# Kernel tuning notes

Measured on AMD Instinct MI355X. Metric: run time of the kernel, lower is better.

Reference implementation:

```python
import jax, jax.numpy as jnp
import numpy as np

B, L, H, C = 32, 2048, 512, 50
KERNEL = 3  # avgpool kernel, stride 1, pad 1, count_include_pad=False


def _avgpool3_no_pad_count(x):
    """AvgPool1d(kernel=3, stride=1, pad=1, count_include_pad=False) along last axis.
    x: (..., L). Zero-pad, sum 3-tap windows, divide by number of valid elements."""
    pad = [(0, 0)] * (x.ndim - 1) + [(1, 1)]
    xp = jnp.pad(x, pad)
    s = xp[..., :-2] + xp[..., 1:-1] + xp[..., 2:]
    ones = jnp.pad(jnp.ones_like(x), pad)
    cnt = ones[..., :-2] + ones[..., 1:-1] + ones[..., 2:]
    return s / cnt


def setup_inputs() -> dict:
    key = jax.random.key(0)
    k1, k2, k3, k4, k5, k6 = jax.random.split(key, 6)
    sent_keys = jax.random.normal(k1, (B, L, H), dtype=jnp.float32)
    sent_values = jax.random.normal(k2, (B, L, H), dtype=jnp.float32)
    sent_lens = jax.random.randint(k3, (B,), 1, L + 1).astype(jnp.int64)
    W1 = jax.random.normal(k4, (H, H), dtype=jnp.float32) * 0.02
    W2 = jax.random.normal(k5, (H, H), dtype=jnp.float32) * 0.02
    W3 = jax.random.normal(k6, (C, H), dtype=jnp.float32) * 0.02
    return {"sent_keys": sent_keys, "sent_values": sent_values,
            "sent_lens": sent_lens, "W1": W1, "W2": W2, "W3": W3}


def reference(sent_keys, sent_values, sent_lens, W1, W2, W3):
    # Tiny MLP scorer (dropout is identity in eval mode)
    p1 = jnp.tanh(jnp.einsum('blh,kh->blk', sent_keys, W1))   # (B,L,H)
    p2 = jnp.tanh(jnp.einsum('blh,kh->blk', p1, W2))          # (B,L,H)
    p3 = jnp.einsum('blh,ch->blc', p1 + p2, W3)               # (B,L,C)

    b, l, c = p3.shape
    # Fill padded positions with the score at the last valid position (index len-1)
    last_idx = (sent_lens - 1).astype(jnp.int32)[:, None, None]        # (B,1,1)
    last = jnp.take_along_axis(p3, jnp.broadcast_to(last_idx, (b, 1, c)), axis=1)  # (B,1,C)
    mask = (jnp.arange(l)[None, :] < sent_lens[:, None])[:, :, None]   # (B,L,1)
    kq = jnp.where(mask, p3, last)

    # Smooth along doc-position axis with avgpool(count_include_pad=False)
    smoothened_kq = _avgpool3_no_pad_count(kq.transpose(0, 2, 1)).transpose(0, 2, 1)  # (B,L,C)

    # Softmax over classes, then zero out padded positions
    attention_values = jax.nn.softmax(smoothened_kq, axis=2)
    attention_values = jnp.where(mask, attention_values, 0.0)

    # (B,C,L) @ (B,L,H) -> (B,C,H)
    class_inputs = jnp.einsum('blc,blh->bch', attention_values, sent_values)
    return attention_values, class_inputs, smoothened_kq
```

## Files before the change

### kernel.cpp

```cpp
#include <hip/hip_runtime.h>
#include <cstdint>

#define Bc 32
#define Lc 2048
#define Hc 512
#define Cc 50
#define PCc 52
#define Mc (Bc*Lc)

typedef short s8v   __attribute__((ext_vector_type(8)));
typedef float f4v   __attribute__((ext_vector_type(4)));

__device__ inline unsigned short f2bf(float f) {
    unsigned int u = __float_as_uint(f);
    u += 0x7fffu + ((u >> 16) & 1u);
    return (unsigned short)(u >> 16);
}
__device__ inline float bf2f(unsigned short h) {
    return __uint_as_float(((unsigned int)h) << 16);
}
__device__ inline float fast_tanh(float x) {
    float e = __expf(2.0f * x);
    return 1.0f - 2.0f / (e + 1.0f);
}
__device__ inline void gl_lds16(const unsigned short* g, unsigned short* l) {
    __builtin_amdgcn_global_load_lds(
        (const __attribute__((address_space(1))) unsigned int*)g,
        (__attribute__((address_space(3))) unsigned int*)l, 16, 0, 0);
}

__global__ __launch_bounds__(256)
void f32_to_bf16_kernel(const float* __restrict__ in, unsigned short* __restrict__ out)
{
    size_t i = ((size_t)blockIdx.x * 256 + threadIdx.x) * 8;
    float4 a = *(const float4*)(in + i);
    float4 b = *(const float4*)(in + i + 4);
    s8v o;
    o[0]=f2bf(a.x); o[1]=f2bf(a.y); o[2]=f2bf(a.z); o[3]=f2bf(a.w);
    o[4]=f2bf(b.x); o[5]=f2bf(b.y); o[6]=f2bf(b.z); o[7]=f2bf(b.w);
    *(s8v*)(out + i) = o;
}

__global__ __launch_bounds__(256)
void convert_weights_kernel(const float* __restrict__ W1, const float* __restrict__ W2,
                            const float* __restrict__ W3,
                            unsigned short* __restrict__ W1b,
                            unsigned short* __restrict__ W2b,
                            unsigned short* __restrict__ W3b)
{
    int e = (blockIdx.x * 256 + threadIdx.x) * 8;
    if (e >= 524288) {
        int off = e - 524288;
        int row = off >> 9;
        s8v o;
        #pragma unroll
        for (int j = 0; j < 8; ++j)
            o[j] = (row < Cc) ? (short)f2bf(W3[off + j]) : (short)0;
        *(s8v*)(W3b + off) = o;
        return;
    }
    const float* src = (e < 262144) ? W1 : W2;
    unsigned short* dst = (e < 262144) ? W1b : W2b;
    int off = (e < 262144) ? e : e - 262144;
    float4 a = *(const float4*)(src + off);
    float4 b = *(const float4*)(src + off + 4);
    s8v o;
    o[0]=f2bf(a.x); o[1]=f2bf(a.y); o[2]=f2bf(a.z); o[3]=f2bf(a.w);
    o[4]=f2bf(b.x); o[5]=f2bf(b.y); o[6]=f2bf(b.z); o[7]=f2bf(b.w);
    *(s8v*)(dst + off) = o;
}

__global__ __launch_bounds__(256)
void transpose_v_kernel(const float* __restrict__ V, unsigned short* __restrict__ Vt)
{
    __shared__ float tile[64 * 65];
    const int l0 = blockIdx.x * 64;
    const int h0 = blockIdx.y * 64;
    const int b  = blockIdx.z;
    const int tid = threadIdx.x;
    const int li = tid >> 2;
    const int hq = (tid & 3) * 4;

    const float* src = V + ((size_t)(b * Lc + l0 + li)) * Hc + h0 + hq;
    #pragma unroll
    for (int j = 0; j < 4; ++j) {
        float4 v = *(const float4*)(src + 16 * j);
        float* d = &tile[li * 65 + hq + 16 * j];
        d[0] = v.x; d[1] = v.y; d[2] = v.z; d[3] = v.w;
    }
    __syncthreads();

    const int lane = tid & 63;
    const int w4   = tid >> 6;
    const int lpos = (lane & 15) * 4;
    #pragma unroll
    for (int i = 0; i < 4; ++i) {
        int hr = i * 16 + w4 * 4 + (lane >> 4);
        ushort4 o;
        o.x = f2bf(tile[(lpos + 0) * 65 + hr]);
        o.y = f2bf(tile[(lpos + 1) * 65 + hr]);
        o.z = f2bf(tile[(lpos + 2) * 65 + hr]);
        o.w = f2bf(tile[(lpos + 3) * 65 + hr]);
        *(ushort4*)(Vt + ((size_t)(b * Hc + h0 + hr)) * Lc + l0 + lpos) = o;
    }
}

__global__ __launch_bounds__(256)
void mfma_gemm512(const unsigned short* __restrict__ Ab,
                  const unsigned short* __restrict__ Wb,
                  unsigned short* __restrict__ Ob, int mode)
{
    __shared__ alignas(16) char smem[32768];
    float* Esf = (float*)smem;

    const int tid = threadIdx.x;
    const int w = tid >> 6, l = tid & 63;

    const int bid = blockIdx.x;
    const int ixd = bid >> 3;
    const int y   = (bid & 7) * 64 + (ixd >> 2);
    const int x   = ixd & 3;
    const int j0 = x * 128;
    const int i0 = y * 128;

    const int sr  = w * 16 + (l >> 2);
    const int kg8 = (l & 3) * 8;
    const unsigned short* Ag0 = Ab + (size_t)(i0 + sr) * 512 + kg8;
    const unsigned short* Ag1 = Ag0 + (size_t)64 * 512;
    const unsigned short* Bg0 = Wb + (size_t)(j0 + sr) * 512 + kg8;
    const unsigned short* Bg1 = Bg0 + (size_t)64 * 512;

    const int wm = (w & 1) * 64, wn = (w >> 1) * 64;
    const int fr = l & 15;
    const int fq = (l >> 4) * 8;

    f4v acc[4][4];
    #pragma unroll
    for (int r = 0; r < 4; ++r)
        #pragma unroll
        for (int c = 0; c < 4; ++c) acc[r][c] = (f4v){0.f, 0.f, 0.f, 0.f};

    auto STAGE = [&](int buf, int k0) {
        unsigned short* a = (unsigned short*)(smem + buf * 16384);
        unsigned short* b = (unsigned short*)(smem + 8192 + buf * 16384);
        gl_lds16(Ag0 + k0, a + w * 512);
        gl_lds16(Ag1 + k0, a + 2048 + w * 512);
        gl_lds16(Bg0 + k0, b + w * 512);
        gl_lds16(Bg1 + k0, b + 2048 + w * 512);
    };
    auto COMPUTE = [&](int buf) {
        const unsigned short* a = (const unsigned short*)(smem + buf * 16384);
        const unsigned short* b = (const unsigned short*)(smem + 8192 + buf * 16384);
        s8v af[4], bv[4];
        #pragma unroll
        for (int r = 0; r < 4; ++r)
            af[r] = *(const s8v*)&a[(wm + r * 16 + fr) * 32 + fq];
        #pragma unroll
        for (int c = 0; c < 4; ++c)
            bv[c] = *(const s8v*)&b[(wn + c * 16 + fr) * 32 + fq];
        #pragma unroll
        for (int r = 0; r < 4; ++r)
            #pragma unroll
            for (int c = 0; c < 4; ++c)
                acc[r][c] = __builtin_amdgcn_mfma_f32_16x16x32_bf16(
                    af[r], bv[c], acc[r][c], 0, 0, 0);
    };

    STAGE(0, 0);
    #pragma unroll
    for (int t = 0; t < 15; ++t) {
        STAGE((t + 1) & 1, (t + 1) * 32);
        asm volatile("s_waitcnt vmcnt(4)" ::: "memory");
        __builtin_amdgcn_s_barrier();
        COMPUTE(t & 1);
        asm volatile("s_waitcnt lgkmcnt(0)" ::: "memory");
        __builtin_amdgcn_s_barrier();
    }
    asm volatile("s_waitcnt vmcnt(0)" ::: "memory");
    __builtin_amdgcn_s_barrier();
    COMPUTE(1);
    asm volatile("s_waitcnt lgkmcnt(0)" ::: "memory");
    __builtin_amdgcn_s_barrier();

    #pragma unroll
    for (int h = 0; h < 4; ++h) {
        if (h) __syncthreads();
        if ((w & 1) == (h >> 1)) {
            const int rr = (h & 1) * 2;
            #pragma unroll
            for (int r = 0; r < 2; ++r)
                #pragma unroll
                for (int c = 0; c < 4; ++c)
                    #pragma unroll
                    for (int v = 0; v < 4; ++v) {
                        int row = r * 16 + (l >> 4) * 4 + v;
                        int col = wn + c * 16 + fr;
                        Esf[row * 133 + col] = fast_tanh(acc[rr + r][c][v]);
                    }
        }
        __syncthreads();
        #pragma unroll
        for (int t = 0; t < 4; ++t) {
            int chunk = t * 256 + tid;
            int row = chunk >> 5;
            int c4  = (chunk & 31) * 4;
            f4v val = *(const f4v*)&Esf[row * 133 + c4];
            size_t gr   = (size_t)(i0 + (h >> 1) * 64 + (h & 1) * 32 + row);
            size_t goff = gr * 512 + j0 + c4;
            ushort4 o;
            if (mode) {
                ushort4 a = *(const ushort4*)(Ab + goff);
                o.x = f2bf(val[0] + bf2f(a.x));
                o.y = f2bf(val[1] + bf2f(a.y));
                o.z = f2bf(val[2] + bf2f(a.z));
                o.w = f2bf(val[3] + bf2f(a.w));
            } else {
                o.x = f2bf(val[0]); o.y = f2bf(val[1]);
                o.z = f2bf(val[2]); o.w = f2bf(val[3]);
            }
            *(ushort4*)(Ob + goff) = o;
        }
    }
}

__global__ __launch_bounds__(256)
void mfma_gemm_p3(const unsigned short* __restrict__ Sb,
                  const unsigned short* __restrict__ W3b,
                  float* __restrict__ P3)
{
    __shared__ alignas(16) char smem[24576];
    const int tid = threadIdx.x;
    const int w = tid >> 6, l = tid & 63;
    const int i0 = blockIdx.x * 128;

    const int sr  = w * 16 + (l >> 2);
    const int kg8 = (l & 3) * 8;
    const unsigned short* Ag0 = Sb + (size_t)(i0 + sr) * 512 + kg8;
    const unsigned short* Ag1 = Ag0 + (size_t)64 * 512;
    const unsigned short* Bg  = W3b + (size_t)sr * 512 + kg8;

    const int wm = w * 32;
    const int fr = l & 15;
    const int fq = (l >> 4) * 8;

    f4v acc[2][4];
    #pragma unroll
    for (int r = 0; r < 2; ++r)
        #pragma unroll
        for (int c = 0; c < 4; ++c) acc[r][c] = (f4v){0.f, 0.f, 0.f, 0.f};

    auto STAGE = [&](int buf, int k0) {
        unsigned short* a = (unsigned short*)(smem + buf * 12288);
        unsigned short* b = (unsigned short*)(smem + 8192 + buf * 12288);
        gl_lds16(Ag0 + k0, a + w * 512);
        gl_lds16(Ag1 + k0, a + 2048 + w * 512);
        gl_lds16(Bg  + k0, b + w * 512);
    };
    auto COMPUTE = [&](int buf) {
        const unsigned short* a = (const unsigned short*)(smem + buf * 12288);
        const unsigned short* b = (const unsigned short*)(smem + 8192 + buf * 12288);
        s8v af[2], bv[4];
        #pragma unroll
        for (int r = 0; r < 2; ++r)
            af[r] = *(const s8v*)&a[(wm + r * 16 + fr) * 32 + fq];
        #pragma unroll
        for (int c = 0; c < 4; ++c)
            bv[c] = *(const s8v*)&b[(c * 16 + fr) * 32 + fq];
        #pragma unroll
        for (int r = 0; r < 2; ++r)
            #pragma unroll
            for (int c = 0; c < 4; ++c)
                acc[r][c] = __builtin_amdgcn_mfma_f32_16x16x32_bf16(
                    af[r], bv[c], acc[r][c], 0, 0, 0);
    };

    STAGE(0, 0);
    #pragma unroll
    for (int t = 0; t < 15; ++t) {
        STAGE((t + 1) & 1, (t + 1) * 32);
        asm volatile("s_waitcnt vmcnt(3)" ::: "memory");
        __builtin_amdgcn_s_barrier();
        COMPUTE(t & 1);
        asm volatile("s_waitcnt lgkmcnt(0)" ::: "memory");
        __builtin_amdgcn_s_barrier();
    }
    asm volatile("s_waitcnt vmcnt(0)" ::: "memory");
    __builtin_amdgcn_s_barrier();
    COMPUTE(1);

    #pragma unroll
    for (int r = 0; r < 2; ++r)
        #pragma unroll
        for (int v = 0; v < 4; ++v) {
            const int row = i0 + wm + r * 16 + (l >> 4) * 4 + v;
            #pragma unroll
            for (int c = 0; c < 4; ++c) {
                const int col = c * 16 + fr;
                if (col < Cc) P3[(size_t)row * PCc + col] = acc[r][c][v];
            }
        }
}

__global__ __launch_bounds__(64)
void normalize_lens_kernel(const int* __restrict__ raw, int* __restrict__ lens)
{
    __shared__ int is64;
    if (threadIdx.x == 0) {
        int orv = 0;
        for (int i = 1; i < 32; i += 2) orv |= raw[i];
        is64 = (orv == 0) ? 1 : 0;
    }
    __syncthreads();
    int b = threadIdx.x;
    if (b < Bc) lens[b] = is64 ? raw[2*b] : raw[b];
}

__global__ __launch_bounds__(256)
void pool_softmax_kernel(const float* __restrict__ P3, const int* __restrict__ lens,
                         float* __restrict__ out_attn, float* __restrict__ out_smooth,
                         unsigned short* __restrict__ attnT)
{
    const int idx = blockIdx.x * 256 + threadIdx.x;
    const int b = idx >> 11;
    const int l = idx & (Lc - 1);
    const int len = lens[b];
    const float* base = P3 + (size_t)b * Lc * PCc;

    const int  r0 = min(l, len - 1);
    const bool hm = (l > 0);
    const bool hp = (l < Lc - 1);
    const int  rm = hm ? min(l - 1, len - 1) : 0;
    const int  rp = hp ? min(l + 1, len - 1) : 0;
    const float rcnt = 1.f / (1.f + (hm ? 1.f : 0.f) + (hp ? 1.f : 0.f));

    float sm[PCc];
    const float* p0 = base + (size_t)r0 * PCc;
    #pragma unroll
    for (int q = 0; q < 13; ++q) {
        f4v v = *(const f4v*)(p0 + q * 4);
        sm[q*4+0] = v[0]; sm[q*4+1] = v[1]; sm[q*4+2] = v[2]; sm[q*4+3] = v[3];
    }
    if (hm) {
        const float* p = base + (size_t)rm * PCc;
        #pragma unroll
        for (int q = 0; q < 13; ++q) {
            f4v v = *(const f4v*)(p + q * 4);
            sm[q*4+0] += v[0]; sm[q*4+1] += v[1]; sm[q*4+2] += v[2]; sm[q*4+3] += v[3];
        }
    }
    if (hp) {
        const float* p = base + (size_t)rp * PCc;
        #pragma unroll
        for (int q = 0; q < 13; ++q) {
            f4v v = *(const f4v*)(p + q * 4);
            sm[q*4+0] += v[0]; sm[q*4+1] += v[1]; sm[q*4+2] += v[2]; sm[q*4+3] += v[3];
        }
    }

    float mx = -1e30f;
    #pragma unroll
    for (int c = 0; c < Cc; ++c) {
        sm[c] *= rcnt;
        mx = fmaxf(mx, sm[c]);
    }
    float* srow = out_smooth + (size_t)idx * Cc;
    #pragma unroll
    for (int q = 0; q < 25; ++q) {
        float2 v = make_float2(sm[q*2], sm[q*2+1]);
        *(float2*)(srow + q * 2) = v;
    }

    float sum = 0.f;
    #pragma unroll
    for (int c = 0; c < Cc; ++c) {
        float e = __expf(sm[c] - mx);
        sm[c] = e;
        sum += e;
    }
    const float inv = 1.f / sum;
    const bool valid = (l < len);
    const float scale = valid ? inv : 0.f;
    float* arow = out_attn + (size_t)idx * Cc;
    unsigned short* trow = attnT + (size_t)b * 64 * Lc + l;
    #pragma unroll
    for (int c = 0; c < Cc; ++c) sm[c] *= scale;
    #pragma unroll
    for (int q = 0; q < 25; ++q)
        *(float2*)(arow + q * 2) = make_float2(sm[q*2], sm[q*2+1]);
    #pragma unroll
    for (int c = 0; c < Cc; ++c)
        trow[(size_t)c * Lc] = f2bf(sm[c]);
}

__global__ __launch_bounds__(256)
void class_mfma_kernel(const unsigned short* __restrict__ attnT,
                       const unsigned short* __restrict__ Vt,
                       float* __restrict__ out_class)
{
    __shared__ alignas(16) unsigned short As[64 * 32];
    __shared__ alignas(16) unsigned short Bs[128 * 32];
    const int tid = threadIdx.x;
    const int w = tid >> 6, l = tid & 63;

    const int bid  = blockIdx.x;
    const int ixd  = bid >> 3;
    const int pair = (bid & 7) * 16 + (ixd >> 2);
    const int n0 = (ixd & 3) * 128;
    const int b  = pair >> 2;
    const int kb = (pair & 3) * 512;

    const int sr  = w * 16 + (l >> 2);
    const int kg8 = (l & 3) * 8;
    const unsigned short* Ag  = attnT + ((size_t)b * 64 + sr) * Lc + kg8;
    const unsigned short* Bg0 = Vt + ((size_t)(b * Hc + n0 + sr)) * Lc + kg8;
    const unsigned short* Bg1 = Bg0 + (size_t)64 * Lc;
    unsigned short* Al  = As + w * 512;
    unsigned short* Bl0 = Bs + w * 512;
    unsigned short* Bl1 = Bs + 2048 + w * 512;

    const int fr = l & 15;
    const int fq = (l >> 4) * 8;

    f4v acc[4][2];
    #pragma unroll
    for (int r = 0; r < 4; ++r)
        #pragma unroll
        for (int c = 0; c < 2; ++c) acc[r][c] = (f4v){0.f, 0.f, 0.f, 0.f};

    for (int k0 = kb; k0 < kb + 512; k0 += 32) {
        gl_lds16(Ag + k0, Al);
        gl_lds16(Bg0 + k0, Bl0);
        gl_lds16(Bg1 + k0, Bl1);
        __syncthreads();
        s8v af[4], bv[2];
        #pragma unroll
        for (int r = 0; r < 4; ++r)
            af[r] = *(const s8v*)&As[(r * 16 + fr) * 32 + fq];
        #pragma unroll
        for (int c = 0; c < 2; ++c)
            bv[c] = *(const s8v*)&Bs[(w * 32 + c * 16 + fr) * 32 + fq];
        #pragma unroll
        for (int r = 0; r < 4; ++r)
            #pragma unroll
            for (int c = 0; c < 2; ++c)
                acc[r][c] = __builtin_amdgcn_mfma_f32_16x16x32_bf16(
                    af[r], bv[c], acc[r][c], 0, 0, 0);
        __syncthreads();
    }

    #pragma unroll
    for (int r = 0; r < 4; ++r)
        #pragma unroll
        for (int v = 0; v < 4; ++v) {
            const int m = r * 16 + (l >> 4) * 4 + v;
            if (m < Cc) {
                #pragma unroll
                for (int c = 0; c < 2; ++c) {
                    const int h = n0 + w * 32 + c * 16 + fr;
                    atomicAdd(out_class + ((size_t)b * Cc + m) * Hc + h,
                              acc[r][c][v]);
                }
            }
        }
}

extern "C" void kernel_launch(void* const* d_in, const int* in_sizes, int n_in,
                              void* d_out, int out_size, void* d_ws, size_t ws_size,
                              hipStream_t stream)
{
    const float* keys     = (const float*)d_in[0];
    const float* vals     = (const float*)d_in[1];
    const int*   lens_raw = (const int*)d_in[2];
    const float* W1       = (const float*)d_in[3];
    const float* W2       = (const float*)d_in[4];
    const float* W3       = (const float*)d_in[5];

    char* ws = (char*)d_ws;
    const size_t MB = 1024 * 1024;
    unsigned short* Akv  = (unsigned short*)ws;
    float*          P3   = (float*)ws;
    unsigned short* P1b  = (unsigned short*)(ws + 64 * MB);
    unsigned short* Vt   = (unsigned short*)(ws + 64 * MB);
    unsigned short* Sb   = (unsigned short*)(ws + 128 * MB);
    unsigned short* W1b  = (unsigned short*)(ws + 192 * MB);
    unsigned short* W2b  = W1b + Hc * Hc;
    unsigned short* W3b  = W2b + Hc * Hc;
    unsigned short* attnT= (unsigned short*)(ws + 194 * MB);
    int*            lens = (int*)(ws + 202 * MB);

    float* out_attn   = (float*)d_out;
    float* out_class  = out_attn + (size_t)Bc * Lc * Cc;
    float* out_smooth = out_class + (size_t)Bc * Cc * Hc;

    hipMemsetAsync(out_class, 0, (size_t)Bc * Cc * Hc * sizeof(float), stream);

    f32_to_bf16_kernel<<<(Mc * Hc / 8) / 256, 256, 0, stream>>>(keys, Akv);
    convert_weights_kernel<<<272, 256, 0, stream>>>(W1, W2, W3, W1b, W2b, W3b);
    normalize_lens_kernel<<<1, 64, 0, stream>>>(lens_raw, lens);

    mfma_gemm512<<<2048, 256, 0, stream>>>(Akv, W1b, P1b, 0);
    mfma_gemm512<<<2048, 256, 0, stream>>>(P1b, W2b, Sb, 1);
    transpose_v_kernel<<<dim3(Lc / 64, Hc / 64, Bc), 256, 0, stream>>>(vals, Vt);
    mfma_gemm_p3<<<Mc / 128, 256, 0, stream>>>(Sb, W3b, P3);
    pool_softmax_kernel<<<Mc / 256, 256, 0, stream>>>(P3, lens, out_attn, out_smooth, attnT);
    class_mfma_kernel<<<512, 256, 0, stream>>>(attnT, Vt, out_class);
}
```

Baseline: 507.4 us.

## Replace double-buffered K pipeline with single-buffered 64-wide K steps in GEMMs

The two MLP GEMM kernels drop their hand-scheduled double-buffered pipeline (manual vmcnt/lgkmcnt waits and raw barriers). Each now loads a 64-wide K chunk as two 32-wide halves into one buffer, syncs, computes both halves, and syncs again. The class GEMM also moves from 32-wide to 64-wide K steps, halving its barrier count. This trades global-load/compute overlap in the MLP GEMMs for simpler code and fewer barriers per unit of K, and may expose load latency there.

```diff
diff --git a/kernel.cpp b/kernel.cpp
--- a/kernel.cpp
+++ b/kernel.cpp
@@ -111,6 +111,8 @@
                   unsigned short* __restrict__ Ob, int mode)
 {
     __shared__ alignas(16) char smem[32768];
+    unsigned short* As = (unsigned short*)smem;
+    unsigned short* Bs = (unsigned short*)(smem + 16384);
     float* Esf = (float*)smem;
 
     const int tid = threadIdx.x;
@@ -140,47 +142,33 @@
         #pragma unroll
         for (int c = 0; c < 4; ++c) acc[r][c] = (f4v){0.f, 0.f, 0.f, 0.f};
 
-    auto STAGE = [&](int buf, int k0) {
-        unsigned short* a = (unsigned short*)(smem + buf * 16384);
-        unsigned short* b = (unsigned short*)(smem + 8192 + buf * 16384);
-        gl_lds16(Ag0 + k0, a + w * 512);
-        gl_lds16(Ag1 + k0, a + 2048 + w * 512);
-        gl_lds16(Bg0 + k0, b + w * 512);
-        gl_lds16(Bg1 + k0, b + 2048 + w * 512);
-    };
-    auto COMPUTE = [&](int buf) {
-        const unsigned short* a = (const unsigned short*)(smem + buf * 16384);
-        const unsigned short* b = (const unsigned short*)(smem + 8192 + buf * 16384);
-        s8v af[4], bv[4];
-        #pragma unroll
-        for (int r = 0; r < 4; ++r)
-            af[r] = *(const s8v*)&a[(wm + r * 16 + fr) * 32 + fq];
-        #pragma unroll
-        for (int c = 0; c < 4; ++c)
-            bv[c] = *(const s8v*)&b[(wn + c * 16 + fr) * 32 + fq];
-        #pragma unroll
-        for (int r = 0; r < 4; ++r)
+    for (int k0 = 0; k0 < 512; k0 += 64) {
+        #pragma unroll
+        for (int h = 0; h < 2; ++h) {
+            gl_lds16(Ag0 + k0 + h * 32, As + h * 4096 + w * 512);
+            gl_lds16(Ag1 + k0 + h * 32, As + h * 4096 + 2048 + w * 512);
+            gl_lds16(Bg0 + k0 + h * 32, Bs + h * 4096 + w * 512);
+            gl_lds16(Bg1 + k0 + h * 32, Bs + h * 4096 + 2048 + w * 512);
+        }
+        __syncthreads();
+        #pragma unroll
+        for (int h = 0; h < 2; ++h) {
+            s8v af[4], bv[4];
+            #pragma unroll
+            for (int r = 0; r < 4; ++r)
+                af[r] = *(const s8v*)&As[h * 4096 + (wm + r * 16 + fr) * 32 + fq];
             #pragma unroll
             for (int c = 0; c < 4; ++c)
-                acc[r][c] = __builtin_amdgcn_mfma_f32_16x16x32_bf16(
-                    af[r], bv[c], acc[r][c], 0, 0, 0);
-    };
-
-    STAGE(0, 0);
-    #pragma unroll
-    for (int t = 0; t < 15; ++t) {
-        STAGE((t + 1) & 1, (t + 1) * 32);
-        asm volatile("s_waitcnt vmcnt(4)" ::: "memory");
-        __builtin_amdgcn_s_barrier();
-        COMPUTE(t & 1);
-        asm volatile("s_waitcnt lgkmcnt(0)" ::: "memory");
-        __builtin_amdgcn_s_barrier();
-    }
-    asm volatile("s_waitcnt vmcnt(0)" ::: "memory");
-    __builtin_amdgcn_s_barrier();
-    COMPUTE(1);
-    asm volatile("s_waitcnt lgkmcnt(0)" ::: "memory");
-    __builtin_amdgcn_s_barrier();
+                bv[c] = *(const s8v*)&Bs[h * 4096 + (wn + c * 16 + fr) * 32 + fq];
+            #pragma unroll
+            for (int r = 0; r < 4; ++r)
+                #pragma unroll
+                for (int c = 0; c < 4; ++c)
+                    acc[r][c] = __builtin_amdgcn_mfma_f32_16x16x32_bf16(
+                        af[r], bv[c], acc[r][c], 0, 0, 0);
+        }
+        __syncthreads();
+    }
 
     #pragma unroll
     for (int h = 0; h < 4; ++h) {
@@ -229,6 +217,9 @@
                   float* __restrict__ P3)
 {
     __shared__ alignas(16) char smem[24576];
+    unsigned short* As = (unsigned short*)smem;
+    unsigned short* Bs = (unsigned short*)(smem + 16384);
+
     const int tid = threadIdx.x;
     const int w = tid >> 6, l = tid & 63;
     const int i0 = blockIdx.x * 128;
@@ -249,44 +240,32 @@
         #pragma unroll
         for (int c = 0; c < 4; ++c) acc[r][c] = (f4v){0.f, 0.f, 0.f, 0.f};
 
-    auto STAGE = [&](int buf, int k0) {
-        unsigned short* a = (unsigned short*)(smem + buf * 12288);
-        unsigned short* b = (unsigned short*)(smem + 8192 + buf * 12288);
-        gl_lds16(Ag0 + k0, a + w * 512);
-        gl_lds16(Ag1 + k0, a + 2048 + w * 512);
-        gl_lds16(Bg  + k0, b + w * 512);
-    };
-    auto COMPUTE = [&](int buf) {
-        const unsigned short* a = (const unsigned short*)(smem + buf * 12288);
-        const unsigned short* b = (const unsigned short*)(smem + 8192 + buf * 12288);
-        s8v af[2], bv[4];
-        #pragma unroll
-        for (int r = 0; r < 2; ++r)
-            af[r] = *(const s8v*)&a[(wm + r * 16 + fr) * 32 + fq];
-        #pragma unroll
-        for (int c = 0; c < 4; ++c)
-            bv[c] = *(const s8v*)&b[(c * 16 + fr) * 32 + fq];
-        #pragma unroll
-        for (int r = 0; r < 2; ++r)
+    for (int k0 = 0; k0 < 512; k0 += 64) {
+        #pragma unroll
+        for (int h = 0; h < 2; ++h) {
+            gl_lds16(Ag0 + k0 + h * 32, As + h * 4096 + w * 512);
+            gl_lds16(Ag1 + k0 + h * 32, As + h * 4096 + 2048 + w * 512);
+            gl_lds16(Bg  + k0 + h * 32, Bs + h * 2048 + w * 512);
+        }
+        __syncthreads();
+        #pragma unroll
+        for (int h = 0; h < 2; ++h) {
+            s8v af[2], bv[4];
+            #pragma unroll
+            for (int r = 0; r < 2; ++r)
+                af[r] = *(const s8v*)&As[h * 4096 + (wm + r * 16 + fr) * 32 + fq];
             #pragma unroll
             for (int c = 0; c < 4; ++c)
-                acc[r][c] = __builtin_amdgcn_mfma_f32_16x16x32_bf16(
-                    af[r], bv[c], acc[r][c], 0, 0, 0);
-    };
-
-    STAGE(0, 0);
-    #pragma unroll
-    for (int t = 0; t < 15; ++t) {
-        STAGE((t + 1) & 1, (t + 1) * 32);
-        asm volatile("s_waitcnt vmcnt(3)" ::: "memory");
-        __builtin_amdgcn_s_barrier();
-        COMPUTE(t & 1);
-        asm volatile("s_waitcnt lgkmcnt(0)" ::: "memory");
-        __builtin_amdgcn_s_barrier();
-    }
-    asm volatile("s_waitcnt vmcnt(0)" ::: "memory");
-    __builtin_amdgcn_s_barrier();
-    COMPUTE(1);
+                bv[c] = *(const s8v*)&Bs[h * 2048 + (c * 16 + fr) * 32 + fq];
+            #pragma unroll
+            for (int r = 0; r < 2; ++r)
+                #pragma unroll
+                for (int c = 0; c < 4; ++c)
+                    acc[r][c] = __builtin_amdgcn_mfma_f32_16x16x32_bf16(
+                        af[r], bv[c], acc[r][c], 0, 0, 0);
+        }
+        __syncthreads();
+    }
 
     #pragma unroll
     for (int r = 0; r < 2; ++r)
@@ -397,8 +376,10 @@
                        const unsigned short* __restrict__ Vt,
                        float* __restrict__ out_class)
 {
-    __shared__ alignas(16) unsigned short As[64 * 32];
-    __shared__ alignas(16) unsigned short Bs[128 * 32];
+    __shared__ alignas(16) char smem[24576];
+    unsigned short* As = (unsigned short*)smem;
+    unsigned short* Bs = (unsigned short*)(smem + 8192);
+
     const int tid = threadIdx.x;
     const int w = tid >> 6, l = tid & 63;
 
@@ -414,9 +395,6 @@
     const unsigned short* Ag  = attnT + ((size_t)b * 64 + sr) * Lc + kg8;
     const unsigned short* Bg0 = Vt + ((size_t)(b * Hc + n0 + sr)) * Lc + kg8;
     const unsigned short* Bg1 = Bg0 + (size_t)64 * Lc;
-    unsigned short* Al  = As + w * 512;
-    unsigned short* Bl0 = Bs + w * 512;
-    unsigned short* Bl1 = Bs + 2048 + w * 512;
 
     const int fr = l & 15;
     const int fq = (l >> 4) * 8;
@@ -427,24 +405,30 @@
         #pragma unroll
         for (int c = 0; c < 2; ++c) acc[r][c] = (f4v){0.f, 0.f, 0.f, 0.f};
 
-    for (int k0 = kb; k0 < kb + 512; k0 += 32) {
-        gl_lds16(Ag + k0, Al);
-        gl_lds16(Bg0 + k0, Bl0);
-        gl_lds16(Bg1 + k0, Bl1);
-        __syncthreads();
-        s8v af[4], bv[2];
-        #pragma unroll
-        for (int r = 0; r < 4; ++r)
-            af[r] = *(const s8v*)&As[(r * 16 + fr) * 32 + fq];
-        #pragma unroll
-        for (int c = 0; c < 2; ++c)
-            bv[c] = *(const s8v*)&Bs[(w * 32 + c * 16 + fr) * 32 + fq];
-        #pragma unroll
-        for (int r = 0; r < 4; ++r)
+    for (int k0 = kb; k0 < kb + 512; k0 += 64) {
+        #pragma unroll
+        for (int h = 0; h < 2; ++h) {
+            gl_lds16(Ag  + k0 + h * 32, As + h * 2048 + w * 512);
+            gl_lds16(Bg0 + k0 + h * 32, Bs + h * 4096 + w * 512);
+            gl_lds16(Bg1 + k0 + h * 32, Bs + h * 4096 + 2048 + w * 512);
+        }
+        __syncthreads();
+        #pragma unroll
+        for (int h = 0; h < 2; ++h) {
+            s8v af[4], bv[2];
+            #pragma unroll
+            for (int r = 0; r < 4; ++r)
+                af[r] = *(const s8v*)&As[h * 2048 + (r * 16 + fr) * 32 + fq];
             #pragma unroll
             for (int c = 0; c < 2; ++c)
-                acc[r][c] = __builtin_amdgcn_mfma_f32_16x16x32_bf16(
-                    af[r], bv[c], acc[r][c], 0, 0, 0);
+                bv[c] = *(const s8v*)&Bs[h * 4096 + (w * 32 + c * 16 + fr) * 32 + fq];
+            #pragma unroll
+            for (int r = 0; r < 4; ++r)
+                #pragma unroll
+                for (int c = 0; c < 2; ++c)
+                    acc[r][c] = __builtin_amdgcn_mfma_f32_16x16x32_bf16(
+                        af[r], bv[c], acc[r][c], 0, 0, 0);
+        }
         __syncthreads();
     }
 
```

After: 517.9 us. 1.02x slower.
